# Performance work log

Measured on AMD Instinct MI355X. Metric: run time of the kernel, lower is better.

## Reference

```python
import jax, jax.numpy as jnp
import numpy as np

B, C, H, W = 8, 256, 64, 64
EPS = 1e-5


def _mk_conv_bn(key, oc, ic):
    k = jax.random.split(key, 6)
    return dict(
        w=jax.random.normal(k[0], (oc, ic), jnp.float32) * 0.01,  # trunc-normal approx, stddev 0.01
        b=jnp.zeros((oc,), jnp.float32),
        s=jax.random.uniform(k[1], (oc,), jnp.float32, 0.5, 1.5),   # BN scale
        t=jax.random.normal(k[2], (oc,), jnp.float32) * 0.1,        # BN shift
        m=jax.random.normal(k[3], (oc,), jnp.float32) * 0.1,        # BN running mean
        v=jax.random.uniform(k[4], (oc,), jnp.float32, 0.5, 1.5),   # BN running var
    )


def setup_inputs() -> dict:
    key = jax.random.key(0)
    ks = jax.random.split(key, 6)
    d = {"x": jax.random.normal(ks[0], (B, C, H, W), jnp.float32)}
    for i, (oc, ic) in zip([1, 2, 3, 4], [(C // 8, C), (C // 8, C), (C // 2, C), (C, C // 2)]):
        p = _mk_conv_bn(ks[i], oc, ic)
        for name, val in p.items():
            d[f"{name}{i}"] = val
    d["gamma"] = jnp.asarray(0.5, jnp.float32)
    return d


def _cbn(x, w, b, s, t, m, v, relu=True):
    # conv1x1 + BatchNorm(eval) [+ ReLU]; dropout is identity at inference
    y = jnp.einsum('bchw,oc->bohw', x, w) + b[None, :, None, None]
    scale = (s / jnp.sqrt(v + EPS))[None, :, None, None]
    y = (y - m[None, :, None, None]) * scale + t[None, :, None, None]
    return jax.nn.relu(y) if relu else y


def _maxpool2(x):
    b, c, h, w = x.shape
    return x.reshape(b, c, h // 2, 2, w // 2, 2).max(axis=(3, 5))


def reference(x, w1, b1, s1, t1, m1, v1, w2, b2, s2, t2, m2, v2,
              w3, b3, s3, t3, m3, v3, w4, b4, s4, t4, m4, v4, gamma):
    b, c, h, w = x.shape
    f = _maxpool2(_cbn(x, w1, b1, s1, t1, m1, v1))   # (B, C/8, H/2, W/2)
    g = _cbn(x, w2, b2, s2, t2, m2, v2)              # (B, C/8, H, W)
    hh = _maxpool2(_cbn(x, w3, b3, s3, t3, m3, v3))  # (B, C/2, H/2, W/2)
    hw, hw4 = h * w, (h // 2) * (w // 2)
    f = f.reshape(b, c // 8, hw4).transpose(0, 2, 1)  # (B, HW/4, C/8)
    g = g.reshape(b, c // 8, hw)                      # (B, C/8, HW)
    s = jnp.einsum('bnk,bkm->bnm', f, g)              # (B, HW/4, HW)
    beta = jax.nn.softmax(s, axis=1)                  # softmax over dim=1, as in source
    hh = hh.reshape(b, c // 2, hw4)                   # (B, C/2, HW/4)
    o = jnp.einsum('bcn,bnm->bcm', hh, beta).reshape(b, c // 2, h, w)
    out = _cbn(o, w4, b4, s4, t4, m4, v4, relu=False)
    return gamma * out + x
```

## Files before the change

### kernel.cpp

```cpp
#include <hip/hip_runtime.h>
#include <hip/hip_bf16.h>

#define HW   4096
#define HW4  1024
#define EPS  1e-5f
#define SM_SHIFT 20.0f

typedef __attribute__((ext_vector_type(8)))  short    bf16x8;
typedef __attribute__((ext_vector_type(4)))  float    f32x4;

__device__ __forceinline__ short f2bs(float f) {
    union { float f; unsigned u; } v; v.f = f;
    unsigned r = v.u + 0x7FFFu + ((v.u >> 16) & 1u);
    return (short)(r >> 16);
}
__device__ __forceinline__ int swz64(int r, int c)  { return (r << 6) + ((c ^ (r & 7))  << 3); }
__device__ __forceinline__ int swz128(int r, int c) { return (r << 7) + ((c ^ (r & 15)) << 3); }
__device__ __forceinline__ int p40(int r, int c)    { return r * 40 + c * 8; }

__device__ __forceinline__ void bar_lgk() {
    asm volatile("s_waitcnt lgkmcnt(0)" ::: "memory");
    __builtin_amdgcn_s_barrier();
    __builtin_amdgcn_sched_barrier(0);
}

__global__ __launch_bounds__(512) void conv123pool(
    const float* __restrict__ x,
    const float* __restrict__ w1, const float* __restrict__ b1, const float* __restrict__ s1,
    const float* __restrict__ t1, const float* __restrict__ m1, const float* __restrict__ v1,
    const float* __restrict__ w2, const float* __restrict__ b2, const float* __restrict__ s2,
    const float* __restrict__ t2, const float* __restrict__ m2, const float* __restrict__ v2,
    const float* __restrict__ w3, const float* __restrict__ b3, const float* __restrict__ s3,
    const float* __restrict__ t3, const float* __restrict__ m3, const float* __restrict__ v3,
    const float* __restrict__ w4,
    short* __restrict__ w4T,
    short* __restrict__ gbufT, short* __restrict__ fbufT, short* __restrict__ hhbuf)
{
    __shared__ __align__(16) short Wl[4 * 192 * 64];
    __shared__ __align__(16) short Xl[2 * 128 * 64];
    __shared__ float alB[192], beB[192];

    const int t = threadIdx.x;
    const int lane = t & 63, wv = t >> 6;
    const int quad = lane >> 4, l16 = lane & 15;
    const int ptile = blockIdx.x;
    const int bz    = blockIdx.y;
    const int pBase = ptile * 128;
    const int wcol  = (wv & 1) * 32;
    const int woch  = (wv >> 1) * 48;

    const int xp2 = (t & 63) * 2, xkg = t >> 6;
    const float* xBase = x + ((size_t)bz * 256 + xkg * 8) * HW + pBase + xp2;

    float2 fvA[8], fvB[8];
    #pragma unroll
    for (int j = 0; j < 8; ++j) fvA[j] = *(const float2*)(xBase + (size_t)j * HW);

    if (bz == 0) {
        int idx = (ptile * 512 + t) * 2;
        float2 a = *(const float2*)(w4 + idx);
        short2 o; o.x = f2bs(a.x); o.y = f2bs(a.y);
        *(short2*)&w4T[idx] = o;
    }

    if (t < 192) {
        int j = t;
        float pb, ps, ptv, pm, pv;
        if (j < 32)      { pb = b1[j]; ps = s1[j]; ptv = t1[j]; pm = m1[j]; pv = v1[j]; }
        else if (j < 64) { int c = j - 32; pb = b2[c]; ps = s2[c]; ptv = t2[c]; pm = m2[c]; pv = v2[c]; }
        else             { int c = j - 64; pb = b3[c]; ps = s3[c]; ptv = t3[c]; pm = m3[c]; pv = v3[c]; }
        float al = ps * rsqrtf(pv + EPS);
        alB[t] = al; beB[t] = (pb - pm) * al + ptv;
    }

    #pragma unroll
    for (int kc = 0; kc < 4; ++kc) {
        #pragma unroll
        for (int i = 0; i < 2; ++i) {
            int idx = t + i * 512;
            if (i == 0 || t < 256) {
                int oc = idx >> 2, kb = (idx & 3) * 16;
                const float* wp = (oc < 32) ? (w1 + oc * 256)
                                : (oc < 64) ? (w2 + (oc - 32) * 256)
                                            : (w3 + (oc - 64) * 256);
                wp += kc * 64 + kb;
                float4 a = *(const float4*)(wp);
                float4 b = *(const float4*)(wp + 4);
                float4 c = *(const float4*)(wp + 8);
                float4 d = *(const float4*)(wp + 12);
                bf16x8 lo, hi;
                lo[0]=f2bs(a.x); lo[1]=f2bs(a.y); lo[2]=f2bs(a.z); lo[3]=f2bs(a.w);
                lo[4]=f2bs(b.x); lo[5]=f2bs(b.y); lo[6]=f2bs(b.z); lo[7]=f2bs(b.w);
                hi[0]=f2bs(c.x); hi[1]=f2bs(c.y); hi[2]=f2bs(c.z); hi[3]=f2bs(c.w);
                hi[4]=f2bs(d.x); hi[5]=f2bs(d.y); hi[6]=f2bs(d.z); hi[7]=f2bs(d.w);
                *(bf16x8*)&Wl[kc * 12288 + swz64(oc, (kb >> 3))]     = lo;
                *(bf16x8*)&Wl[kc * 12288 + swz64(oc, (kb >> 3) + 1)] = hi;
            }
        }
    }

    const f32x4 fzero = {0.f, 0.f, 0.f, 0.f};
    f32x4 acc[3][4];
    #pragma unroll
    for (int i = 0; i < 3; ++i)
        #pragma unroll
        for (int j = 0; j < 4; ++j) acc[i][j] = fzero;

    const int ptOff0 = wcol, ptOff1 = wcol + 16, ptOff2 = wcol + 64, ptOff3 = wcol + 80;

#define K1_COMMIT(XB, CUR)                                                            \
    {   bf16x8 va, vb;                                                                \
        _Pragma("unroll")                                                             \
        for (int j2 = 0; j2 < 8; ++j2) { va[j2] = f2bs(CUR[j2].x); vb[j2] = f2bs(CUR[j2].y); } \
        *(bf16x8*)&Xl[(XB) * 8192 + swz64(xp2,     xkg)] = va;                        \
        *(bf16x8*)&Xl[(XB) * 8192 + swz64(xp2 + 1, xkg)] = vb;                        \
    }
#define K1_PREF(KC, NXT)                                                              \
    {   const float* xn = xBase + (size_t)((KC) * 64) * HW;                           \
        _Pragma("unroll")                                                             \
        for (int j2 = 0; j2 < 8; ++j2) NXT[j2] = *(const float2*)(xn + (size_t)j2 * HW); \
    }
#define K1_MFMA(XB, KC)                                                               \
    _Pragma("unroll")                                                                 \
    for (int kk = 0; kk < 2; ++kk) {                                                  \
        bf16x8 bfr[4];                                                                \
        bfr[0] = *(const bf16x8*)&Xl[(XB) * 8192 + swz64(ptOff0 + l16, kk * 4 + quad)]; \
        bfr[1] = *(const bf16x8*)&Xl[(XB) * 8192 + swz64(ptOff1 + l16, kk * 4 + quad)]; \
        bfr[2] = *(const bf16x8*)&Xl[(XB) * 8192 + swz64(ptOff2 + l16, kk * 4 + quad)]; \
        bfr[3] = *(const bf16x8*)&Xl[(XB) * 8192 + swz64(ptOff3 + l16, kk * 4 + quad)]; \
        _Pragma("unroll")                                                             \
        for (int tt = 0; tt < 3; ++tt) {                                              \
            bf16x8 afr = *(const bf16x8*)&Wl[(KC) * 12288 + swz64(woch + tt*16 + l16, kk*4 + quad)]; \
            _Pragma("unroll")                                                         \
            for (int pt = 0; pt < 4; ++pt)                                            \
                acc[tt][pt] = __builtin_amdgcn_mfma_f32_16x16x32_bf16(afr, bfr[pt], acc[tt][pt], 0, 0, 0); \
        }                                                                             \
    }

    K1_COMMIT(0, fvA)  K1_PREF(1, fvB)  bar_lgk();  K1_MFMA(0, 0)
    K1_COMMIT(1, fvB)  K1_PREF(2, fvA)  bar_lgk();  K1_MFMA(1, 1)
    K1_COMMIT(0, fvA)  K1_PREF(3, fvB)  bar_lgk();  K1_MFMA(0, 2)
    K1_COMMIT(1, fvB)                   bar_lgk();  K1_MFMA(1, 3)

#undef K1_COMMIT
#undef K1_PREF
#undef K1_MFMA

    #pragma unroll
    for (int tt = 0; tt < 3; ++tt) {
        #pragma unroll
        for (int r = 0; r < 4; ++r) {
            int j = woch + tt * 16 + quad * 4 + r;
            float al = alB[j], be = beB[j];
            float y[4];
            y[0] = fmaxf(acc[tt][0][r] * al + be, 0.f);
            y[1] = fmaxf(acc[tt][1][r] * al + be, 0.f);
            y[2] = fmaxf(acc[tt][2][r] * al + be, 0.f);
            y[3] = fmaxf(acc[tt][3][r] * al + be, 0.f);
            if (j >= 32 && j < 64) {
                size_t mb = (size_t)bz * 4096 + pBase;
                int kk = j - 32;
                gbufT[(mb + ptOff0 + l16) * 32 + kk] = f2bs(y[0]);
                gbufT[(mb + ptOff1 + l16) * 32 + kk] = f2bs(y[1]);
                gbufT[(mb + ptOff2 + l16) * 32 + kk] = f2bs(y[2]);
                gbufT[(mb + ptOff3 + l16) * 32 + kk] = f2bs(y[3]);
            } else {
                #pragma unroll
                for (int c = 0; c < 2; ++c) {
                    float v  = fmaxf(y[c], y[c + 2]);
                    float po = fmaxf(v, __shfl_xor(v, 1));
                    if ((l16 & 1) == 0) {
                        int col = wcol + c * 16 + l16;
                        int n = ptile * 32 + (col >> 1);
                        if (j < 32) fbufT[((size_t)bz * 1024 + n) * 32 + j] = f2bs(po);
                        else        hhbuf[((size_t)bz * 128 + (j - 64)) * HW4 + n] = f2bs(po);
                    }
                }
            }
        }
    }
}

__global__ __launch_bounds__(256, 2) void attn_conv4(
    const short* __restrict__ gbufT,
    const short* __restrict__ fbufT,
    const short* __restrict__ hhbuf,
    const float* __restrict__ x,
    const short* __restrict__ w4T, const float* __restrict__ b4, const float* __restrict__ s4,
    const float* __restrict__ t4, const float* __restrict__ m4, const float* __restrict__ v4,
    const float* __restrict__ gamma, float* __restrict__ out)
{
    __shared__ __align__(16) short smem[24576];
    __shared__ float alB4[256], beB4[256];
    __shared__ float Zl[64];
    short* sT0  = smem;
    short* sT1  = smem + 4096;
    short* hhl0 = smem + 8192;
    short* hhl1 = smem + 16384;
    short* o_l  = smem;
    short* Wl4  = smem + 8192;

    const int t = threadIdx.x;
    const int lane = t & 63, wv = t >> 6;
    const int quad = lane >> 4, l16 = lane & 15;
    const int bz = blockIdx.y;
    const int m0 = blockIdx.x * 64;
    const f32x4 fzero = {0.f, 0.f, 0.f, 0.f};

    {
        float al = s4[t] * rsqrtf(v4[t] + EPS);
        alB4[t] = al; beB4[t] = (b4[t] - m4[t]) * al + t4[t];
    }

    const short* fT = fbufT + (size_t)bz * 1024 * 32;
    const short* hB = hhbuf + (size_t)bz * 128 * HW4;
    const int hrow = t >> 3, hnc = t & 7;

    bf16x8 bg = *(const bf16x8*)&gbufT[((size_t)bz * 4096 + m0 + wv * 16 + l16) * 32 + quad * 8];

    bf16x8 fr[4], hr[4];
    #pragma unroll
    for (int nt = 0; nt < 4; ++nt)
        fr[nt] = *(const bf16x8*)&fT[(nt * 16 + l16) * 32 + quad * 8];
    #pragma unroll
    for (int i = 0; i < 4; ++i)
        hr[i] = *(const bf16x8*)(hB + (size_t)(i * 32 + hrow) * HW4 + hnc * 8);

    float psum = 0.f;
    f32x4 oacc[2][4];
    #pragma unroll
    for (int a = 0; a < 2; ++a)
        #pragma unroll
        for (int b = 0; b < 4; ++b) oacc[a][b] = fzero;

    #pragma unroll 2
    for (int it = 0; it < 16; ++it) {
        const int n0n = ((it + 1) & 15) << 6;
        short* hb = (it & 1) ? hhl1 : hhl0;
        short* sT = (it & 1) ? sT1  : sT0;

        #pragma unroll
        for (int i = 0; i < 4; ++i)
            *(bf16x8*)&hb[swz64(i * 32 + hrow, hnc)] = hr[i];
        #pragma unroll
        for (int i = 0; i < 4; ++i)
            hr[i] = *(const bf16x8*)(hB + (size_t)(i * 32 + hrow) * HW4 + n0n + hnc * 8);

        f32x4 sacc[4];
        #pragma unroll
        for (int nt = 0; nt < 4; ++nt)
            sacc[nt] = __builtin_amdgcn_mfma_f32_16x16x32_bf16(fr[nt], bg, fzero, 0, 0, 0);
        #pragma unroll
        for (int nt = 0; nt < 4; ++nt)
            fr[nt] = *(const bf16x8*)&fT[(n0n + nt * 16 + l16) * 32 + quad * 8];

        #pragma unroll
        for (int nt = 0; nt < 4; ++nt) {
            short4 ev;
            #pragma unroll
            for (int r = 0; r < 4; ++r) {
                float e = __expf(sacc[nt][r] - SM_SHIFT);
                psum += e;
                ((short*)&ev)[r] = f2bs(e);
            }
            *(short4*)&sT[swz64(wv * 16 + l16, nt * 2 + (quad >> 1)) + (quad & 1) * 4] = ev;
        }

        bar_lgk();

        #pragma unroll
        for (int kk = 0; kk < 2; ++kk) {
            bf16x8 ah0 = *(const bf16x8*)&hb[swz64(wv * 32 + l16,      kk * 4 + quad)];
            bf16x8 ah1 = *(const bf16x8*)&hb[swz64(wv * 32 + 16 + l16, kk * 4 + quad)];
            bf16x8 bs[4];
            #pragma unroll
            for (int mt = 0; mt < 4; ++mt)
                bs[mt] = *(const bf16x8*)&sT[swz64(mt * 16 + l16, kk * 4 + quad)];
            #pragma unroll
            for (int mt = 0; mt < 4; ++mt) {
                oacc[0][mt] = __builtin_amdgcn_mfma_f32_16x16x32_bf16(ah0, bs[mt], oacc[0][mt], 0, 0, 0);
                oacc[1][mt] = __builtin_amdgcn_mfma_f32_16x16x32_bf16(ah1, bs[mt], oacc[1][mt], 0, 0, 0);
            }
        }
    }

    psum += __shfl_xor(psum, 16);
    psum += __shfl_xor(psum, 32);
    if (quad == 0) Zl[wv * 16 + l16] = psum;
    bar_lgk();

    #pragma unroll
    for (int mt = 0; mt < 4; ++mt) {
        float iv = 1.0f / Zl[mt * 16 + l16];
        #pragma unroll
        for (int ct2 = 0; ct2 < 2; ++ct2) {
            short4 ov;
            #pragma unroll
            for (int r = 0; r < 4; ++r) ((short*)&ov)[r] = f2bs(oacc[ct2][mt][r] * iv);
            *(short4*)&o_l[swz128(mt * 16 + l16, wv * 4 + ct2 * 2 + (quad >> 1)) + (quad & 1) * 4] = ov;
        }
    }

    f32x4 acc4[4][4];
    #pragma unroll
    for (int i = 0; i < 4; ++i)
        #pragma unroll
        for (int j = 0; j < 4; ++j) acc4[i][j] = fzero;

    const int wrow = t >> 2, wcid = t & 3;
    bf16x8 Wr[4];
    #pragma unroll
    for (int g = 0; g < 4; ++g)
        Wr[g] = *(const bf16x8*)(w4T + (g * 64 + wrow) * 128 + wcid * 8);

    #pragma unroll
    for (int k0i = 0; k0i < 4; ++k0i) {
        const int k0 = k0i * 32;
        bar_lgk();
        #pragma unroll
        for (int g = 0; g < 4; ++g)
            *(bf16x8*)&Wl4[p40(g * 64 + wrow, wcid)] = Wr[g];
        if (k0i < 3) {
            #pragma unroll
            for (int g = 0; g < 4; ++g)
                Wr[g] = *(const bf16x8*)(w4T + (g * 64 + wrow) * 128 + k0 + 32 + wcid * 8);
        }
        bar_lgk();
        bf16x8 bfr[4];
        #pragma unroll
        for (int mt = 0; mt < 4; ++mt)
            bfr[mt] = *(const bf16x8*)&o_l[swz128(mt * 16 + l16, (k0 >> 3) + quad)];
        #pragma unroll
        for (int ot = 0; ot < 4; ++ot) {
            bf16x8 afr = *(const bf16x8*)&Wl4[p40(wv * 64 + ot * 16 + l16, quad)];
            #pragma unroll
            for (int mt = 0; mt < 4; ++mt)
                acc4[ot][mt] = __builtin_amdgcn_mfma_f32_16x16x32_bf16(afr, bfr[mt], acc4[ot][mt], 0, 0, 0);
        }
    }

    float gm = gamma[0];
    #pragma unroll
    for (int ot = 0; ot < 4; ++ot) {
        #pragma unroll
        for (int r = 0; r < 4; ++r) {
            int oc = wv * 64 + ot * 16 + quad * 4 + r;
            float al = alB4[oc], be = beB4[oc];
            #pragma unroll
            for (int mt = 0; mt < 4; ++mt) {
                int p = m0 + mt * 16 + l16;
                float y  = acc4[ot][mt][r] * al + be;
                float xo = x[((size_t)bz * 256 + oc) * HW + p];
                out[((size_t)bz * 256 + oc) * HW + p] = gm * y + xo;
            }
        }
    }
}

extern "C" void kernel_launch(void* const* d_in, const int* in_sizes, int n_in,
                              void* d_out, int out_size, void* d_ws, size_t ws_size,
                              hipStream_t stream)
{
    const float* x  = (const float*)d_in[0];
    const float* w1 = (const float*)d_in[1];
    const float* b1 = (const float*)d_in[2];
    const float* s1 = (const float*)d_in[3];
    const float* t1 = (const float*)d_in[4];
    const float* m1 = (const float*)d_in[5];
    const float* v1 = (const float*)d_in[6];
    const float* w2 = (const float*)d_in[7];
    const float* b2 = (const float*)d_in[8];
    const float* s2 = (const float*)d_in[9];
    const float* t2 = (const float*)d_in[10];
    const float* m2 = (const float*)d_in[11];
    const float* v2 = (const float*)d_in[12];
    const float* w3 = (const float*)d_in[13];
    const float* b3 = (const float*)d_in[14];
    const float* s3 = (const float*)d_in[15];
    const float* t3 = (const float*)d_in[16];
    const float* m3 = (const float*)d_in[17];
    const float* v3 = (const float*)d_in[18];
    const float* w4 = (const float*)d_in[19];
    const float* b4 = (const float*)d_in[20];
    const float* s4 = (const float*)d_in[21];
    const float* t4 = (const float*)d_in[22];
    const float* m4 = (const float*)d_in[23];
    const float* v4 = (const float*)d_in[24];
    const float* gm = (const float*)d_in[25];
    float* out = (float*)d_out;

    short* gbufT = (short*)d_ws;
    short* fbufT = gbufT + (size_t)8 * 4096 * 32;
    short* hhbuf = fbufT + (size_t)8 * 1024 * 32;
    short* w4T   = hhbuf + (size_t)8 * 128 * 1024;

    conv123pool<<<dim3(32, 8), 512, 0, stream>>>(
        x, w1, b1, s1, t1, m1, v1, w2, b2, s2, t2, m2, v2, w3, b3, s3, t3, m3, v3,
        w4, w4T, gbufT, fbufT, hhbuf);
    attn_conv4<<<dim3(64, 8), 256, 0, stream>>>(
        gbufT, fbufT, hhbuf, x, w4T, b4, s4, t4, m4, v4, gm, out);
}
```

Baseline: 162.0 us.

## Split attention K dimension across waves to remove per-iteration block barriers

```diff
diff --git a/kernel.cpp b/kernel.cpp
--- a/kernel.cpp
+++ b/kernel.cpp
@@ -13,6 +13,11 @@
     union { float f; unsigned u; } v; v.f = f;
     unsigned r = v.u + 0x7FFFu + ((v.u >> 16) & 1u);
     return (short)(r >> 16);
+}
+__device__ __forceinline__ unsigned pk2(float a, float b) {
+    unsigned r;
+    asm("v_cvt_pk_bf16_f32 %0, %1, %2" : "=v"(r) : "v"(a), "v"(b));
+    return r;
 }
 __device__ __forceinline__ int swz64(int r, int c)  { return (r << 6) + ((c ^ (r & 7))  << 3); }
 __device__ __forceinline__ int swz128(int r, int c) { return (r << 7) + ((c ^ (r & 15)) << 3); }
@@ -192,17 +197,17 @@
 {
     __shared__ __align__(16) short smem[24576];
     __shared__ float alB4[256], beB4[256];
-    __shared__ float Zl[64];
-    short* sT0  = smem;
-    short* sT1  = smem + 4096;
-    short* hhl0 = smem + 8192;
-    short* hhl1 = smem + 16384;
+    __shared__ float Zl[128];
     short* o_l  = smem;
     short* Wl4  = smem + 8192;
+    float* mrg  = (float*)(smem + 8192);
+    short* sTp  = smem + (threadIdx.x >> 6) * 2560;
 
     const int t = threadIdx.x;
     const int lane = t & 63, wv = t >> 6;
     const int quad = lane >> 4, l16 = lane & 15;
+    const int ci = wv >> 1, ni = wv & 1;
+    const int nstrip = ni * 32, cbase = ci * 64;
     const int bz = blockIdx.y;
     const int m0 = blockIdx.x * 64;
     const f32x4 fzero = {0.f, 0.f, 0.f, 0.f};
@@ -214,90 +219,115 @@
 
     const short* fT = fbufT + (size_t)bz * 1024 * 32;
     const short* hB = hhbuf + (size_t)bz * 128 * HW4;
-    const int hrow = t >> 3, hnc = t & 7;
-
-    bf16x8 bg = *(const bf16x8*)&gbufT[((size_t)bz * 4096 + m0 + wv * 16 + l16) * 32 + quad * 8];
-
-    bf16x8 fr[4], hr[4];
-    #pragma unroll
-    for (int nt = 0; nt < 4; ++nt)
-        fr[nt] = *(const bf16x8*)&fT[(nt * 16 + l16) * 32 + quad * 8];
-    #pragma unroll
-    for (int i = 0; i < 4; ++i)
-        hr[i] = *(const bf16x8*)(hB + (size_t)(i * 32 + hrow) * HW4 + hnc * 8);
-
-    float psum = 0.f;
-    f32x4 oacc[2][4];
-    #pragma unroll
-    for (int a = 0; a < 2; ++a)
+
+    bf16x8 bg[4];
+    #pragma unroll
+    for (int mt = 0; mt < 4; ++mt)
+        bg[mt] = *(const bf16x8*)&gbufT[((size_t)bz * 4096 + m0 + mt * 16 + l16) * 32 + quad * 8];
+
+    bf16x8 frA[2], frB[2], hhA[4], hhB[4];
+    frA[0] = *(const bf16x8*)&fT[(size_t)(nstrip + l16) * 32 + quad * 8];
+    frA[1] = *(const bf16x8*)&fT[(size_t)(nstrip + 16 + l16) * 32 + quad * 8];
+    #pragma unroll
+    for (int ct = 0; ct < 4; ++ct)
+        hhA[ct] = *(const bf16x8*)(hB + (size_t)(cbase + ct * 16 + l16) * HW4 + nstrip + quad * 8);
+
+    float psum[4] = {0.f, 0.f, 0.f, 0.f};
+    f32x4 oacc[4][4];
+    #pragma unroll
+    for (int a = 0; a < 4; ++a)
         #pragma unroll
         for (int b = 0; b < 4; ++b) oacc[a][b] = fzero;
 
-    #pragma unroll 2
-    for (int it = 0; it < 16; ++it) {
-        const int n0n = ((it + 1) & 15) << 6;
-        short* hb = (it & 1) ? hhl1 : hhl0;
-        short* sT = (it & 1) ? sT1  : sT0;
-
-        #pragma unroll
-        for (int i = 0; i < 4; ++i)
-            *(bf16x8*)&hb[swz64(i * 32 + hrow, hnc)] = hr[i];
-        #pragma unroll
-        for (int i = 0; i < 4; ++i)
-            hr[i] = *(const bf16x8*)(hB + (size_t)(i * 32 + hrow) * HW4 + n0n + hnc * 8);
-
-        f32x4 sacc[4];
-        #pragma unroll
-        for (int nt = 0; nt < 4; ++nt)
-            sacc[nt] = __builtin_amdgcn_mfma_f32_16x16x32_bf16(fr[nt], bg, fzero, 0, 0, 0);
-        #pragma unroll
-        for (int nt = 0; nt < 4; ++nt)
-            fr[nt] = *(const bf16x8*)&fT[(n0n + nt * 16 + l16) * 32 + quad * 8];
-
-        #pragma unroll
-        for (int nt = 0; nt < 4; ++nt) {
-            short4 ev;
-            #pragma unroll
-            for (int r = 0; r < 4; ++r) {
-                float e = __expf(sacc[nt][r] - SM_SHIFT);
-                psum += e;
-                ((short*)&ev)[r] = f2bs(e);
-            }
-            *(short4*)&sT[swz64(wv * 16 + l16, nt * 2 + (quad >> 1)) + (quad & 1) * 4] = ev;
-        }
-
-        bar_lgk();
-
-        #pragma unroll
-        for (int kk = 0; kk < 2; ++kk) {
-            bf16x8 ah0 = *(const bf16x8*)&hb[swz64(wv * 32 + l16,      kk * 4 + quad)];
-            bf16x8 ah1 = *(const bf16x8*)&hb[swz64(wv * 32 + 16 + l16, kk * 4 + quad)];
-            bf16x8 bs[4];
+    const int mr0 = l16 * 40, mr1 = (16 + l16) * 40, mr2 = (32 + l16) * 40, mr3 = (48 + l16) * 40;
+    const int mrow[4] = {mr0, mr1, mr2, mr3};
+
+    int n0n = 64;
+
+#define ABODY(CURF, NXTF, CURH, NXTH)                                                 \
+    {                                                                                 \
+        f32x4 sacc0[4], sacc1[4];                                                     \
+        _Pragma("unroll")                                                             \
+        for (int mt = 0; mt < 4; ++mt)                                                \
+            sacc0[mt] = __builtin_amdgcn_mfma_f32_16x16x32_bf16(CURF[0], bg[mt], fzero, 0, 0, 0); \
+        _Pragma("unroll")                                                             \
+        for (int mt = 0; mt < 4; ++mt)                                                \
+            sacc1[mt] = __builtin_amdgcn_mfma_f32_16x16x32_bf16(CURF[1], bg[mt], fzero, 0, 0, 0); \
+        NXTF[0] = *(const bf16x8*)&fT[(size_t)(n0n + nstrip + l16) * 32 + quad * 8];  \
+        NXTF[1] = *(const bf16x8*)&fT[(size_t)(n0n + nstrip + 16 + l16) * 32 + quad * 8]; \
+        _Pragma("unroll")                                                             \
+        for (int mt = 0; mt < 4; ++mt) {                                              \
+            float e0 = __expf(sacc0[mt][0] - SM_SHIFT);                               \
+            float e1 = __expf(sacc0[mt][1] - SM_SHIFT);                               \
+            float e2 = __expf(sacc0[mt][2] - SM_SHIFT);                               \
+            float e3 = __expf(sacc0[mt][3] - SM_SHIFT);                               \
+            float g0 = __expf(sacc1[mt][0] - SM_SHIFT);                               \
+            float g1 = __expf(sacc1[mt][1] - SM_SHIFT);                               \
+            float g2 = __expf(sacc1[mt][2] - SM_SHIFT);                               \
+            float g3 = __expf(sacc1[mt][3] - SM_SHIFT);                               \
+            psum[mt] += ((e0 + e1) + (e2 + e3)) + ((g0 + g1) + (g2 + g3));            \
+            uint2 ev0; ev0.x = pk2(e0, e1); ev0.y = pk2(e2, e3);                      \
+            uint2 ev1; ev1.x = pk2(g0, g1); ev1.y = pk2(g2, g3);                      \
+            *(uint2*)&sTp[mrow[mt] + quad * 4]      = ev0;                            \
+            *(uint2*)&sTp[mrow[mt] + 16 + quad * 4] = ev1;                            \
+        }                                                                             \
+        _Pragma("unroll")                                                             \
+        for (int mt = 0; mt < 4; ++mt) {                                              \
+            bf16x8 bfrag = *(const bf16x8*)&sTp[mrow[mt] + quad * 8];                 \
+            _Pragma("unroll")                                                         \
+            for (int ct = 0; ct < 4; ++ct)                                            \
+                oacc[ct][mt] = __builtin_amdgcn_mfma_f32_16x16x32_bf16(CURH[ct], bfrag, oacc[ct][mt], 0, 0, 0); \
+        }                                                                             \
+        _Pragma("unroll")                                                             \
+        for (int ct = 0; ct < 4; ++ct)                                                \
+            NXTH[ct] = *(const bf16x8*)(hB + (size_t)(cbase + ct * 16 + l16) * HW4 + n0n + nstrip + quad * 8); \
+        n0n = (n0n + 64) & 1023;                                                      \
+    }
+
+    for (int it2 = 0; it2 < 8; ++it2) {
+        ABODY(frA, frB, hhA, hhB)
+        ABODY(frB, frA, hhB, hhA)
+    }
+#undef ABODY
+
+    #pragma unroll
+    for (int mt = 0; mt < 4; ++mt) {
+        psum[mt] += __shfl_xor(psum[mt], 16);
+        psum[mt] += __shfl_xor(psum[mt], 32);
+    }
+
+    bar_lgk();
+
+    if (ci == 0 && quad == 0) {
+        #pragma unroll
+        for (int mt = 0; mt < 4; ++mt) Zl[ni * 64 + mt * 16 + l16] = psum[mt];
+    }
+    if (ni == 1) {
+        #pragma unroll
+        for (int ct = 0; ct < 4; ++ct)
             #pragma unroll
             for (int mt = 0; mt < 4; ++mt)
-                bs[mt] = *(const bf16x8*)&sT[swz64(mt * 16 + l16, kk * 4 + quad)];
+                #pragma unroll
+                for (int r = 0; r < 4; ++r)
+                    mrg[(cbase + ct * 16 + quad * 4 + r) * 64 + mt * 16 + l16] = oacc[ct][mt][r];
+    }
+    bar_lgk();
+
+    if (ni == 0) {
+        #pragma unroll
+        for (int mt = 0; mt < 4; ++mt) {
+            float iv = 1.0f / (Zl[mt * 16 + l16] + Zl[64 + mt * 16 + l16]);
             #pragma unroll
-            for (int mt = 0; mt < 4; ++mt) {
-                oacc[0][mt] = __builtin_amdgcn_mfma_f32_16x16x32_bf16(ah0, bs[mt], oacc[0][mt], 0, 0, 0);
-                oacc[1][mt] = __builtin_amdgcn_mfma_f32_16x16x32_bf16(ah1, bs[mt], oacc[1][mt], 0, 0, 0);
+            for (int ct = 0; ct < 4; ++ct) {
+                short4 ov;
+                #pragma unroll
+                for (int r = 0; r < 4; ++r) {
+                    float v = oacc[ct][mt][r]
+                            + mrg[(cbase + ct * 16 + quad * 4 + r) * 64 + mt * 16 + l16];
+                    ((short*)&ov)[r] = f2bs(v * iv);
+                }
+                *(short4*)&o_l[swz128(mt * 16 + l16, ci * 8 + ct * 2 + (quad >> 1)) + (quad & 1) * 4] = ov;
             }
-        }
-    }
-
-    psum += __shfl_xor(psum, 16);
-    psum += __shfl_xor(psum, 32);
-    if (quad == 0) Zl[wv * 16 + l16] = psum;
-    bar_lgk();
-
-    #pragma unroll
-    for (int mt = 0; mt < 4; ++mt) {
-        float iv = 1.0f / Zl[mt * 16 + l16];
-        #pragma unroll
-        for (int ct2 = 0; ct2 < 2; ++ct2) {
-            short4 ov;
-            #pragma unroll
-            for (int r = 0; r < 4; ++r) ((short*)&ov)[r] = f2bs(oacc[ct2][mt][r] * iv);
-            *(short4*)&o_l[swz128(mt * 16 + l16, wv * 4 + ct2 * 2 + (quad >> 1)) + (quad & 1) * 4] = ov;
         }
     }
 
```

New measurement: 164.8 us. About the same (+1.8%).
